# Kernel optimization log

Measured on AMD Instinct MI355X. Metric: run time of the kernel, lower is better.

The kernel has to match this reference:

```python
import jax, jax.numpy as jnp
import numpy as np

NUM_GRAPHS = 256
BN_EPS = 1e-5
GN_EPS = 1e-5


def setup_inputs() -> dict:
    key = jax.random.key(0)
    ks = jax.random.split(key, 8)
    N, E, D, H = 100000, 600000, 128, 128
    x = jax.random.normal(ks[0], (N, D), dtype=jnp.float32)
    W1 = jax.random.normal(ks[1], (4, 4 * H, D), dtype=jnp.float32) * 0.05
    bn_g = jnp.ones((4, 4 * H), dtype=jnp.float32)
    bn_b = jnp.zeros((4, 4 * H), dtype=jnp.float32)
    W2 = jax.random.normal(ks[2], (4, H, 4 * H), dtype=jnp.float32) * 0.05
    b2 = jnp.zeros((4, H), dtype=jnp.float32)
    gn_g = jnp.ones((4, H), dtype=jnp.float32)
    gn_b = jnp.zeros((4, H), dtype=jnp.float32)
    gn_a = jnp.ones((4, H), dtype=jnp.float32)
    edge_index = jax.random.randint(ks[3], (2, E), 0, N, dtype=jnp.int64)
    batch = jnp.sort(jax.random.randint(ks[4], (N,), 0, NUM_GRAPHS, dtype=jnp.int64))
    return {"x": x, "W1": W1, "bn_g": bn_g, "bn_b": bn_b, "W2": W2, "b2": b2,
            "gn_g": gn_g, "gn_b": gn_b, "gn_a": gn_a,
            "edge_index": edge_index, "batch": batch}


def reference(x, W1, bn_g, bn_b, W2, b2, gn_g, gn_b, gn_a, edge_index, batch):
    N = x.shape[0]
    src, dst = edge_index[0], edge_index[1]
    # per-graph node counts (shared by GraphNorm and mean-pool)
    cnt = jax.ops.segment_sum(jnp.ones((N,), x.dtype), batch, num_segments=NUM_GRAPHS)
    cnt = jnp.maximum(cnt, 1.0)[:, None]  # [G,1]

    h = x
    hs = []
    for l in range(4):  # fixed small layer loop
        # GINConv: (1+eps)*x + sum_{j->i} x_j, eps=0 default
        agg = jax.ops.segment_sum(h[src], dst, num_segments=N)
        z = h + agg
        # MLP: Linear(no bias) -> BatchNorm1d (batch stats) -> SELU -> Linear
        z = z @ W1[l].T
        mu = jnp.mean(z, axis=0)
        var = jnp.mean((z - mu) ** 2, axis=0)
        z = (z - mu) * jax.lax.rsqrt(var + BN_EPS) * bn_g[l] + bn_b[l]
        z = jax.nn.selu(z)
        z = z @ W2[l].T + b2[l]
        # GraphNorm: per-graph mean/var with learnable mean scale alpha
        gmean = jax.ops.segment_sum(z, batch, num_segments=NUM_GRAPHS) / cnt
        sub = z - gn_a[l] * gmean[batch]
        gvar = jax.ops.segment_sum(sub * sub, batch, num_segments=NUM_GRAPHS) / cnt
        z = gn_g[l] * sub * jax.lax.rsqrt(gvar[batch] + GN_EPS) + gn_b[l]
        z = jax.nn.selu(z)  # self.act (SELU, matching MLP)
        hs.append(z)
        h = z

    hg = jnp.concatenate(hs, axis=1)  # [N, 4*H]
    pooled = jax.ops.segment_sum(hg, batch, num_segments=NUM_GRAPHS) / cnt
    return pooled
```

## Files before the change

kernel.cpp:

```cpp
#include <hip/hip_runtime.h>
#include <hip/hip_bf16.h>


typedef __attribute__((ext_vector_type(8))) short bf16x8;
typedef __attribute__((ext_vector_type(4))) float f32x4;

#define MOMB 256

__device__ __forceinline__ unsigned short f2b(float x){
    __hip_bfloat16 h = __float2bfloat16(x);
    return *reinterpret_cast<unsigned short*>(&h);
}
__device__ __forceinline__ float b2f(unsigned short u){
    __hip_bfloat16 h;
    *reinterpret_cast<unsigned short*>(&h) = u;
    return __bfloat162float(h);
}
__device__ __forceinline__ float selu_f(float x){
    const float sc = 1.0507009873554805f, al = 1.6732632423543772f;
    return x > 0.f ? sc * x : sc * al * (__expf(x) - 1.f);
}

__global__ void count_kernel(const int* __restrict__ dst, int* __restrict__ counts, int E){
    int e = blockIdx.x * 256 + threadIdx.x;
    if (e < E) atomicAdd(&counts[dst[e]], 1);
}

__global__ void cnt_bs_kernel(const int* __restrict__ batch, float* __restrict__ cnt, int N){
    __shared__ int sb[257];
    int g = threadIdx.x;
    int lo = 0, hi = N;
    while (lo < hi){ int mid = (lo + hi) >> 1; if (batch[mid] < g) lo = mid + 1; else hi = mid; }
    sb[g] = lo;
    if (g == 0) sb[256] = N;
    __syncthreads();
    cnt[g] = fmaxf((float)(sb[g + 1] - sb[g]), 1.f);
}

__global__ __launch_bounds__(1024) void scan_kernel(const int* __restrict__ counts,
                                                    int* __restrict__ row_ptr, int N){
    __shared__ int wsum[16];
    __shared__ int wpre[16];
    __shared__ int s_total;
    __shared__ int s_running;
    int tid = threadIdx.x;
    int lane = tid & 63, wid = tid >> 6;
    if (tid == 0) s_running = 0;
    __syncthreads();
    for (int base = 0; base < N; base += 4096){
        int idx0 = base + tid * 4;
        int v[4];
        #pragma unroll
        for (int j = 0; j < 4; j++) v[j] = (idx0 + j < N) ? counts[idx0 + j] : 0;
        int tsum = v[0] + v[1] + v[2] + v[3];
        int x = tsum;
        #pragma unroll
        for (int off = 1; off < 64; off <<= 1){
            int y = __shfl_up(x, off, 64);
            if (lane >= off) x += y;
        }
        if (lane == 63) wsum[wid] = x;
        __syncthreads();
        if (wid == 0 && lane < 16){
            int w = wsum[lane];
            int xx = w;
            #pragma unroll
            for (int off = 1; off < 16; off <<= 1){
                int y = __shfl_up(xx, off, 64);
                if (lane >= off) xx += y;
            }
            wpre[lane] = xx - w;
            if (lane == 15) s_total = xx;
        }
        __syncthreads();
        int run = s_running + wpre[wid] + (x - tsum);
        #pragma unroll
        for (int j = 0; j < 4; j++){
            if (idx0 + j < N) row_ptr[idx0 + j] = run;
            run += v[j];
        }
        __syncthreads();
        if (tid == 0) s_running += s_total;
        __syncthreads();
    }
    if (tid == 0) row_ptr[N] = s_running;
}

__global__ void fill_kernel(const int* __restrict__ ei, const int* __restrict__ row_ptr,
                            int* __restrict__ fill, int* __restrict__ colv, int E){
    int e = blockIdx.x * 256 + threadIdx.x;
    if (e < E){
        int s = ei[e];
        int d = ei[E + e];
        int pos = atomicAdd(&fill[d], 1);
        colv[row_ptr[d] + pos] = s;
    }
}

__global__ void pack_kernel(const float* __restrict__ W1, const float* __restrict__ W2,
                            unsigned short* __restrict__ W1p, unsigned short* __restrict__ W2p){
    int t = blockIdx.x * 256 + threadIdx.x;
    int which = t >> 15;
    int u = t & 32767;
    int lane = u & 63; u >>= 6;
    int nf = u & 3; u >>= 2;
    int wc = u & 1; u >>= 1;
    int kk = u & 3; u >>= 2;
    int c = u & 3; u >>= 2;
    int l = u;
    int col = wc * 64 + nf * 16 + (lane & 15);
    int kbase = kk * 32 + (lane >> 4) * 8;
    size_t ob = ((((((size_t)(l * 4 + c) * 4 + kk) * 2 + wc) * 4 + nf) * 2) * 512) + lane * 8;
    unsigned short* dst = which == 0 ? W1p : W2p;
    #pragma unroll
    for (int j = 0; j < 8; j++){
        int k = kbase + j;
        float wv = which == 0 ? W1[((size_t)(l * 512) + c * 128 + col) * 128 + k]
                              : W2[((size_t)(l * 128) + col) * 512 + c * 128 + k];
        unsigned short hi = f2b(wv);
        unsigned short lo = f2b(wv - b2f(hi));
        dst[ob + j] = hi;
        dst[ob + 512 + j] = lo;
    }
}

__global__ __launch_bounds__(256) void agg_split_kernel(
    const float* __restrict__ h, const int* __restrict__ row_ptr,
    const int* __restrict__ colv,
    unsigned short* __restrict__ zhi, unsigned short* __restrict__ zlo, int N)
{
    int t = blockIdx.x * 256 + threadIdx.x;
    int i = t >> 5;
    if (i >= N) return;
    int vo = (t & 31);
    const float4* hv = reinterpret_cast<const float4*>(h);
    int p0 = row_ptr[i], p1 = row_ptr[i + 1];
    float4 acc = hv[(size_t)i * 32 + vo];
    int p = p0;
    for (; p + 4 <= p1; p += 4){
        int s0 = colv[p], s1 = colv[p + 1], s2 = colv[p + 2], s3 = colv[p + 3];
        float4 a = hv[(size_t)s0 * 32 + vo];
        float4 b = hv[(size_t)s1 * 32 + vo];
        float4 c = hv[(size_t)s2 * 32 + vo];
        float4 d = hv[(size_t)s3 * 32 + vo];
        acc.x += (a.x + b.x) + (c.x + d.x);
        acc.y += (a.y + b.y) + (c.y + d.y);
        acc.z += (a.z + b.z) + (c.z + d.z);
        acc.w += (a.w + b.w) + (c.w + d.w);
    }
    for (; p < p1; p++){
        float4 a = hv[(size_t)colv[p] * 32 + vo];
        acc.x += a.x; acc.y += a.y; acc.z += a.z; acc.w += a.w;
    }
    float vals[4] = {acc.x, acc.y, acc.z, acc.w};
    unsigned int h01, h23, l01, l23;
    {
        unsigned short hh[4], ll[4];
        #pragma unroll
        for (int j = 0; j < 4; j++){
            hh[j] = f2b(vals[j]);
            ll[j] = f2b(vals[j] - b2f(hh[j]));
        }
        h01 = (unsigned int)hh[0] | ((unsigned int)hh[1] << 16);
        h23 = (unsigned int)hh[2] | ((unsigned int)hh[3] << 16);
        l01 = (unsigned int)ll[0] | ((unsigned int)ll[1] << 16);
        l23 = (unsigned int)ll[2] | ((unsigned int)ll[3] << 16);
    }
    int kk = vo >> 3, kg = (vo >> 1) & 3, half = vo & 1;
    size_t fo = ((size_t)(i >> 4) * 4 + kk) * 512 + (kg * 16 + (i & 15)) * 8 + half * 4;
    *reinterpret_cast<uint2*>(zhi + fo) = make_uint2(h01, h23);
    *reinterpret_cast<uint2*>(zlo + fo) = make_uint2(l01, l23);
}

__device__ __forceinline__ bf16x8 tread(const unsigned short* __restrict__ s, int base){
    union { bf16x8 v; unsigned short u[8]; } r;
    #pragma unroll
    for (int j = 0; j < 8; j++) r.u[j] = s[base + j * 8];
    return r.v;
}

__global__ __launch_bounds__(256) void moment_k(
    const unsigned short* __restrict__ Zhi_g, const unsigned short* __restrict__ Zlo_g,
    float* __restrict__ Mpart, float* __restrict__ cpart, int RB)
{
    __shared__ __align__(16) unsigned short Zh_s[16384];
    __shared__ __align__(16) unsigned short Zl_s[16384];
    __shared__ float cs[256];
    int tid = threadIdx.x, lane = tid & 63, w = tid >> 6;
    int fl = lane & 15, g = lane >> 4;
    int tpart = (g >> 1) * 2048 + (g & 1) * 64;
    int fpart = (fl >> 3) * 128 + (fl & 7);

    f32x4 acc[2][8];
    #pragma unroll
    for (int i = 0; i < 2; i++)
        #pragma unroll
        for (int j = 0; j < 8; j++) acc[i][j] = (f32x4){0.f, 0.f, 0.f, 0.f};
    float csum = 0.f;
    int cf = tid & 127, chalf = tid >> 7;
    int cfbase = (cf >> 5) * 512 + ((cf >> 3) & 3) * 128 + (cf & 7);

    for (int blk = blockIdx.x; blk < RB; blk += MOMB){
        __syncthreads();
        {
            size_t gbase = (size_t)blk * 16384;
            const uint4* gh = reinterpret_cast<const uint4*>(Zhi_g + gbase);
            const uint4* gl = reinterpret_cast<const uint4*>(Zlo_g + gbase);
            uint4* sh4 = reinterpret_cast<uint4*>(Zh_s);
            uint4* sl4 = reinterpret_cast<uint4*>(Zl_s);
            #pragma unroll
            for (int j = 0; j < 8; j++){
                sh4[j * 256 + tid] = gh[j * 256 + tid];
                sl4[j * 256 + tid] = gl[j * 256 + tid];
            }
        }
        __syncthreads();

        #pragma unroll 8
        for (int n = chalf * 64; n < chalf * 64 + 64; n++){
            int addr = (n >> 4) * 2048 + (n & 15) * 8 + cfbase;
            csum += b2f(Zh_s[addr]) + b2f(Zl_s[addr]);
        }

        for (int nk = 0; nk < 4; nk++){
            int nb = nk * 4096 + tpart + fpart;
            bf16x8 ath[2], atl[2];
            #pragma unroll
            for (int i = 0; i < 2; i++){
                int ft = w * 2 + i;
                int base = nb + (ft >> 1) * 512 + (ft & 1) * 256;
                ath[i] = tread(Zh_s, base);
                atl[i] = tread(Zl_s, base);
            }
            #pragma unroll
            for (int ft2 = 0; ft2 < 8; ft2++){
                int base2 = nb + (ft2 >> 1) * 512 + (ft2 & 1) * 256;
                bf16x8 bth = tread(Zh_s, base2);
                bf16x8 btl = tread(Zl_s, base2);
                #pragma unroll
                for (int i = 0; i < 2; i++){
                    acc[i][ft2] = __builtin_amdgcn_mfma_f32_16x16x32_bf16(ath[i], bth, acc[i][ft2], 0, 0, 0);
                    acc[i][ft2] = __builtin_amdgcn_mfma_f32_16x16x32_bf16(ath[i], btl, acc[i][ft2], 0, 0, 0);
                    acc[i][ft2] = __builtin_amdgcn_mfma_f32_16x16x32_bf16(atl[i], bth, acc[i][ft2], 0, 0, 0);
                }
            }
        }
    }

    float* Mp = Mpart + (size_t)blockIdx.x * 16384;
    int col = lane & 15, rbase = (lane >> 4) * 4;
    #pragma unroll
    for (int i = 0; i < 2; i++)
        #pragma unroll
        for (int ft2 = 0; ft2 < 8; ft2++)
            #pragma unroll
            for (int r = 0; r < 4; r++){
                int a = (w * 2 + i) * 16 + rbase + r;
                int b = ft2 * 16 + col;
                Mp[a * 128 + b] = acc[i][ft2][r];
            }
    cs[tid] = csum;
    __syncthreads();
    if (tid < 128) cpart[(size_t)blockIdx.x * 128 + tid] = cs[tid] + cs[tid + 128];
}

__global__ __launch_bounds__(256) void reduce_k(
    const float* __restrict__ Mpart, const float* __restrict__ cpart,
    float* __restrict__ Msum, float* __restrict__ colsum)
{
    int gid = blockIdx.x * 256 + threadIdx.x;
    float s = 0.f;
    for (int p = 0; p < MOMB; p++) s += Mpart[(size_t)p * 16384 + gid];
    Msum[gid] = s;
    if (blockIdx.x == 0 && threadIdx.x < 128){
        float c = 0.f;
        for (int p = 0; p < MOMB; p++) c += cpart[(size_t)p * 128 + threadIdx.x];
        colsum[threadIdx.x] = c;
    }
}

__global__ __launch_bounds__(128) void bn_final2_k(
    const float* __restrict__ Msum, const float* __restrict__ colsum,
    const float* __restrict__ W1, const float* __restrict__ bng,
    const float* __restrict__ bnb, float* __restrict__ sc, float* __restrict__ sh,
    int l, float invN)
{
    __shared__ float s_w[128];
    __shared__ float red[4];
    int j = blockIdx.x;
    int t = threadIdx.x;
    float wt = W1[(size_t)l * 65536 + (size_t)j * 128 + t];
    s_w[t] = wt;
    __syncthreads();
    float y = 0.f;
    #pragma unroll 4
    for (int k = 0; k < 128; k++) y = fmaf(Msum[t * 128 + k], s_w[k], y);
    float p = wt * y;
    float mc = wt * colsum[t];
    #pragma unroll
    for (int off = 32; off >= 1; off >>= 1){
        p += __shfl_xor(p, off, 64);
        mc += __shfl_xor(mc, off, 64);
    }
    int lane = t & 63, wv = t >> 6;
    if (lane == 0){ red[wv * 2] = p; red[wv * 2 + 1] = mc; }
    __syncthreads();
    if (t == 0){
        float e2 = (red[0] + red[2]) * invN;
        float mu = (red[1] + red[3]) * invN;
        float var = e2 - mu * mu;
        float inv = rsqrtf(var + 1e-5f);
        float gg = bng[l * 512 + j] * inv;
        sc[j] = gg;
        sh[j] = bnb[l * 512 + j] - mu * gg;
    }
}

__global__ __launch_bounds__(512, 4) void fused_k(
    const unsigned short* __restrict__ Zhi_g, const unsigned short* __restrict__ Zlo_g,
    const unsigned short* __restrict__ B1p, const unsigned short* __restrict__ B2p,
    float* __restrict__ Z, const float* __restrict__ bsc, const float* __restrict__ bsh,
    const float* __restrict__ b2l, const int* __restrict__ batch,
    float* __restrict__ gsum, float* __restrict__ gsq, int N)
{
    __shared__ __align__(16) unsigned short Zh_s[8192];
    __shared__ __align__(16) unsigned short Zl_s[8192];
    __shared__ __align__(16) unsigned short Ph[64][136];
    __shared__ __align__(16) unsigned short Pl[64][136];
    __shared__ float s_sc[512], s_sh[512];
    __shared__ int s_b[64];
    int tid = threadIdx.x, lane = tid & 63, w = tid >> 6;
    int wr = w >> 2, wq = w & 3;
    int r_lo = lane & 15, kg = lane >> 4;
    int m0 = blockIdx.x * 64;

    if (tid < 512){ s_sc[tid] = bsc[tid]; s_sh[tid] = bsh[tid]; }
    if (tid < 64) s_b[tid] = (m0 + tid < N) ? batch[m0 + tid] : -1;
    {
        size_t gbase = (size_t)(m0 >> 4) * 2048;
        const uint4* gh = reinterpret_cast<const uint4*>(Zhi_g + gbase);
        const uint4* gl = reinterpret_cast<const uint4*>(Zlo_g + gbase);
        uint4* sh4 = reinterpret_cast<uint4*>(Zh_s);
        uint4* sl4 = reinterpret_cast<uint4*>(Zl_s);
        #pragma unroll
        for (int j = 0; j < 2; j++){
            sh4[j * 512 + tid] = gh[j * 512 + tid];
            sl4[j * 512 + tid] = gl[j * 512 + tid];
        }
    }
    __syncthreads();

    int wc = wq >> 1;
    f32x4 acc2[2][2];
    #pragma unroll
    for (int i = 0; i < 2; i++)
        #pragma unroll
        for (int j = 0; j < 2; j++) acc2[i][j] = (f32x4){0.f, 0.f, 0.f, 0.f};

    for (int c = 0; c < 4; c++){
        f32x4 acc1[2][2];
        #pragma unroll
        for (int i = 0; i < 2; i++)
            #pragma unroll
            for (int j = 0; j < 2; j++) acc1[i][j] = (f32x4){0.f, 0.f, 0.f, 0.f};

        const bf16x8* B1v = reinterpret_cast<const bf16x8*>(B1p) + (size_t)c * 4096;
        for (int kk = 0; kk < 4; kk++){
            bf16x8 awh[2], awl[2];
            #pragma unroll
            for (int mfp = 0; mfp < 2; mfp++){
                int colblk = wq * 2 + mfp;
                int wc1 = colblk >> 2, nf1 = colblk & 3;
                int ob = ((kk * 2 + wc1) * 4 + nf1) * 2;
                awh[mfp] = B1v[(ob + 0) * 64 + lane];
                awl[mfp] = B1v[(ob + 1) * 64 + lane];
            }
            bf16x8 bzh[2], bzl[2];
            #pragma unroll
            for (int nfp = 0; nfp < 2; nfp++){
                int so = ((wr * 2 + nfp) * 4 + kk) * 512 + lane * 8;
                bzh[nfp] = *reinterpret_cast<const bf16x8*>(&Zh_s[so]);
                bzl[nfp] = *reinterpret_cast<const bf16x8*>(&Zl_s[so]);
            }
            #pragma unroll
            for (int mfp = 0; mfp < 2; mfp++)
                #pragma unroll
                for (int nfp = 0; nfp < 2; nfp++){
                    acc1[mfp][nfp] = __builtin_amdgcn_mfma_f32_16x16x32_bf16(awh[mfp], bzh[nfp], acc1[mfp][nfp], 0, 0, 0);
                    acc1[mfp][nfp] = __builtin_amdgcn_mfma_f32_16x16x32_bf16(awh[mfp], bzl[nfp], acc1[mfp][nfp], 0, 0, 0);
                    acc1[mfp][nfp] = __builtin_amdgcn_mfma_f32_16x16x32_bf16(awl[mfp], bzh[nfp], acc1[mfp][nfp], 0, 0, 0);
                }
        }

        __syncthreads();
        #pragma unroll
        for (int mfp = 0; mfp < 2; mfp++){
            int ckb = wq * 32 + mfp * 16 + kg * 4;
            float sc0 = s_sc[c * 128 + ckb + 0], sh0 = s_sh[c * 128 + ckb + 0];
            float sc1 = s_sc[c * 128 + ckb + 1], sh1 = s_sh[c * 128 + ckb + 1];
            float sc2 = s_sc[c * 128 + ckb + 2], sh2 = s_sh[c * 128 + ckb + 2];
            float sc3 = s_sc[c * 128 + ckb + 3], sh3 = s_sh[c * 128 + ckb + 3];
            #pragma unroll
            for (int nfp = 0; nfp < 2; nfp++){
                float t0 = selu_f(fmaf(acc1[mfp][nfp][0], sc0, sh0));
                float t1 = selu_f(fmaf(acc1[mfp][nfp][1], sc1, sh1));
                float t2 = selu_f(fmaf(acc1[mfp][nfp][2], sc2, sh2));
                float t3 = selu_f(fmaf(acc1[mfp][nfp][3], sc3, sh3));
                unsigned short h0 = f2b(t0), h1 = f2b(t1), h2 = f2b(t2), h3 = f2b(t3);
                unsigned short l0 = f2b(t0 - b2f(h0)), l1 = f2b(t1 - b2f(h1));
                unsigned short l2 = f2b(t2 - b2f(h2)), l3 = f2b(t3 - b2f(h3));
                int node = wr * 32 + nfp * 16 + r_lo;
                uint2 hv = make_uint2((unsigned int)h0 | ((unsigned int)h1 << 16),
                                      (unsigned int)h2 | ((unsigned int)h3 << 16));
                uint2 lv = make_uint2((unsigned int)l0 | ((unsigned int)l1 << 16),
                                      (unsigned int)l2 | ((unsigned int)l3 << 16));
                *reinterpret_cast<uint2*>(&Ph[node][ckb]) = hv;
                *reinterpret_cast<uint2*>(&Pl[node][ckb]) = lv;
            }
        }
        __syncthreads();

        const bf16x8* B2v = reinterpret_cast<const bf16x8*>(B2p);
        for (int kk2 = 0; kk2 < 4; kk2++){
            int kkf = c * 4 + kk2;
            bf16x8 bh[2], bl[2];
            #pragma unroll
            for (int nf = 0; nf < 2; nf++){
                int nfold = (wq & 1) * 2 + nf;
                int ob = ((kkf * 2 + wc) * 4 + nfold) * 2;
                bh[nf] = B2v[(ob + 0) * 64 + lane];
                bl[nf] = B2v[(ob + 1) * 64 + lane];
            }
            bf16x8 ah[2], alr[2];
            #pragma unroll
            for (int mf = 0; mf < 2; mf++){
                int ar = wr * 32 + mf * 16 + r_lo;
                ah[mf]  = *reinterpret_cast<const bf16x8*>(&Ph[ar][kk2 * 32 + kg * 8]);
                alr[mf] = *reinterpret_cast<const bf16x8*>(&Pl[ar][kk2 * 32 + kg * 8]);
            }
            #pragma unroll
            for (int mf = 0; mf < 2; mf++)
                #pragma unroll
                for (int nf = 0; nf < 2; nf++){
                    acc2[mf][nf] = __builtin_amdgcn_mfma_f32_16x16x32_bf16(ah[mf],  bh[nf], acc2[mf][nf], 0, 0, 0);
                    acc2[mf][nf] = __builtin_amdgcn_mfma_f32_16x16x32_bf16(ah[mf],  bl[nf], acc2[mf][nf], 0, 0, 0);
                    acc2[mf][nf] = __builtin_amdgcn_mfma_f32_16x16x32_bf16(alr[mf], bh[nf], acc2[mf][nf], 0, 0, 0);
                }
        }
    }

    #pragma unroll
    for (int nf = 0; nf < 2; nf++){
        int col = wq * 32 + nf * 16 + r_lo;
        float bv = b2l[col];
        float s = 0.f, q = 0.f;
        int run_g = -2;
        #pragma unroll
        for (int mf = 0; mf < 2; mf++)
            #pragma unroll
            for (int r = 0; r < 4; r++){
                int row_l = wr * 32 + mf * 16 + kg * 4 + r;
                int row = m0 + row_l;
                if (row < N){
                    float v = bv + acc2[mf][nf][r];
                    Z[(size_t)row * 128 + col] = v;
                    int g = s_b[row_l];
                    if (g != run_g){
                        if (run_g >= 0){
                            atomicAdd(&gsum[run_g * 128 + col], s);
                            atomicAdd(&gsq[run_g * 128 + col], q);
                        }
                        s = 0.f; q = 0.f; run_g = g;
                    }
                    s += v; q += v * v;
                }
            }
        if (run_g >= 0){
            atomicAdd(&gsum[run_g * 128 + col], s);
            atomicAdd(&gsq[run_g * 128 + col], q);
        }
    }
}

__global__ void gn_final_kernel(float* __restrict__ gsum, float* __restrict__ gsq,
                                const float* __restrict__ cnt,
                                const float* __restrict__ gng, const float* __restrict__ gnb,
                                const float* __restrict__ gna,
                                float* __restrict__ scale, float* __restrict__ shift, int l){
    int g = blockIdx.x, c = threadIdx.x;
    int idx = g * 128 + c;
    float n = cnt[g];
    float m = gsum[idx] / n;
    float e2 = gsq[idx] / n;
    float a = gna[l * 128 + c];
    float var = e2 - (2.f * a - a * a) * m * m;
    float inv = rsqrtf(var + 1e-5f);
    float sc = gng[l * 128 + c] * inv;
    scale[idx] = sc;
    shift[idx] = gnb[l * 128 + c] - a * m * sc;
    gsum[idx] = 0.f;
    gsq[idx] = 0.f;
}

__global__ __launch_bounds__(256) void gn_apply_kernel(
    float* __restrict__ z2h, const int* __restrict__ batch,
    const float* __restrict__ scale, const float* __restrict__ shift,
    float* __restrict__ pool, int l, int N)
{
    __shared__ int sb[128];
    int tid = threadIdx.x;
    int base = blockIdx.x * 128;
    int end = min(128, N - base);
    if (tid < 128) sb[tid] = (tid < end) ? batch[base + tid] : 0;
    __syncthreads();
    int vo = tid & 31;
    int r0 = (tid >> 5) * 16;
    if (r0 >= end) return;
    int rend = min(r0 + 16, end);
    float4* zv = reinterpret_cast<float4*>(z2h);
    int run_g = sb[r0];
    float scx = scale[run_g * 128 + vo * 4 + 0], shx = shift[run_g * 128 + vo * 4 + 0];
    float scy = scale[run_g * 128 + vo * 4 + 1], shy = shift[run_g * 128 + vo * 4 + 1];
    float scz = scale[run_g * 128 + vo * 4 + 2], shz = shift[run_g * 128 + vo * 4 + 2];
    float scw = scale[run_g * 128 + vo * 4 + 3], shw = shift[run_g * 128 + vo * 4 + 3];
    float px = 0.f, py = 0.f, pz = 0.f, pw = 0.f;
    for (int r = r0; r < rend; r++){
        int g = sb[r];
        if (g != run_g){
            float* pp = &pool[run_g * 512 + l * 128 + vo * 4];
            atomicAdd(pp + 0, px); atomicAdd(pp + 1, py); atomicAdd(pp + 2, pz); atomicAdd(pp + 3, pw);
            px = py = pz = pw = 0.f;
            run_g = g;
            scx = scale[g * 128 + vo * 4 + 0]; shx = shift[g * 128 + vo * 4 + 0];
            scy = scale[g * 128 + vo * 4 + 1]; shy = shift[g * 128 + vo * 4 + 1];
            scz = scale[g * 128 + vo * 4 + 2]; shz = shift[g * 128 + vo * 4 + 2];
            scw = scale[g * 128 + vo * 4 + 3]; shw = shift[g * 128 + vo * 4 + 3];
        }
        size_t idx = (size_t)(base + r) * 32 + vo;
        float4 v = zv[idx];
        v.x = selu_f(fmaf(v.x, scx, shx));
        v.y = selu_f(fmaf(v.y, scy, shy));
        v.z = selu_f(fmaf(v.z, scz, shz));
        v.w = selu_f(fmaf(v.w, scw, shw));
        zv[idx] = v;
        px += v.x; py += v.y; pz += v.z; pw += v.w;
    }
    float* pp = &pool[run_g * 512 + l * 128 + vo * 4];
    atomicAdd(pp + 0, px); atomicAdd(pp + 1, py); atomicAdd(pp + 2, pz); atomicAdd(pp + 3, pw);
}

__global__ void final_kernel(const float* __restrict__ pool, const float* __restrict__ cnt,
                             float* __restrict__ out, int n){
    int i = blockIdx.x * 256 + threadIdx.x;
    if (i < n) out[i] = pool[i] / cnt[i >> 9];
}

extern "C" void kernel_launch(void* const* d_in, const int* in_sizes, int n_in,
                              void* d_out, int out_size, void* d_ws, size_t ws_size,
                              hipStream_t stream){
    const float* x    = (const float*)d_in[0];
    const float* W1   = (const float*)d_in[1];
    const float* bng  = (const float*)d_in[2];
    const float* bnb  = (const float*)d_in[3];
    const float* W2   = (const float*)d_in[4];
    const float* b2   = (const float*)d_in[5];
    const float* gng  = (const float*)d_in[6];
    const float* gnb  = (const float*)d_in[7];
    const float* gna  = (const float*)d_in[8];
    const int*   ei   = (const int*)d_in[9];
    const int*   batch= (const int*)d_in[10];
    int N = in_sizes[0] / 128;
    int E = in_sizes[9] / 2;
    float* out = (float*)d_out;
    int RB = (N + 127) / 128;
    int RB64 = (N + 63) / 64;

    char* ws = (char*)d_ws;
    size_t off = 0;
    auto alloc = [&](size_t bytes) -> char* {
        char* p = ws + off;
        off += (bytes + 255) & ~(size_t)255;
        return p;
    };
    unsigned short* z0hi = (unsigned short*)alloc((size_t)RB * 128 * 128 * 2);
    unsigned short* z0lo = (unsigned short*)alloc((size_t)RB * 128 * 128 * 2);
    float* z2     = (float*)alloc((size_t)N * 128 * 4);
    unsigned short* W1p = (unsigned short*)alloc(524288 * 2);
    unsigned short* W2p = (unsigned short*)alloc(524288 * 2);
    int*   row_ptr= (int*)alloc((size_t)(N + 1) * 4);
    int*   colv   = (int*)alloc((size_t)E * 4);
    int*   counts = (int*)alloc((size_t)N * 4);
    int*   fill   = (int*)alloc((size_t)N * 4);
    float* cnt_f  = (float*)alloc(256 * 4);
    float* Mpart  = (float*)alloc((size_t)MOMB * 16384 * 4);
    float* cpart  = (float*)alloc((size_t)MOMB * 128 * 4);
    float* Msum   = (float*)alloc(16384 * 4);
    float* colsum = (float*)alloc(128 * 4);
    float* bn_sc  = (float*)alloc(512 * 4);
    float* bn_sh  = (float*)alloc(512 * 4);
    float* gn_sum = (float*)alloc(256 * 128 * 4);
    float* gn_sq  = (float*)alloc(256 * 128 * 4);
    float* gn_sc  = (float*)alloc(256 * 128 * 4);
    float* gn_sh  = (float*)alloc(256 * 128 * 4);
    float* pool   = (float*)alloc(256 * 512 * 4);
    (void)ws_size;

    hipMemsetAsync(counts, 0, (size_t)N * 4, stream);
    hipMemsetAsync(fill,   0, (size_t)N * 4, stream);
    hipMemsetAsync(gn_sum, 0, 2 * 256 * 128 * 4, stream);
    hipMemsetAsync(pool,   0, 256 * 512 * 4, stream);
    {
        size_t tail_start = (size_t)(N >> 4) * 2048;
        size_t total      = (size_t)RB * 128 * 128;
        if (total > tail_start){
            size_t tail_bytes = (total - tail_start) * 2;
            hipMemsetAsync(z0hi + tail_start, 0, tail_bytes, stream);
            hipMemsetAsync(z0lo + tail_start, 0, tail_bytes, stream);
        }
    }

    pack_kernel<<<256, 256, 0, stream>>>(W1, W2, W1p, W2p);
    count_kernel<<<(E + 255) / 256, 256, 0, stream>>>(ei + E, counts, E);
    scan_kernel<<<1, 1024, 0, stream>>>(counts, row_ptr, N);
    fill_kernel<<<(E + 255) / 256, 256, 0, stream>>>(ei, row_ptr, fill, colv, E);
    cnt_bs_kernel<<<1, 256, 0, stream>>>(batch, cnt_f, N);

    const float* hcur = x;
    float invN = 1.f / (float)N;
    for (int l = 0; l < 4; l++){
        agg_split_kernel<<<(N + 7) / 8, 256, 0, stream>>>(hcur, row_ptr, colv, z0hi, z0lo, N);
        moment_k<<<MOMB, 256, 0, stream>>>(z0hi, z0lo, Mpart, cpart, RB);
        reduce_k<<<64, 256, 0, stream>>>(Mpart, cpart, Msum, colsum);
        bn_final2_k<<<512, 128, 0, stream>>>(Msum, colsum, W1, bng, bnb,
                                             bn_sc, bn_sh, l, invN);
        fused_k<<<RB64, 512, 0, stream>>>(z0hi, z0lo, W1p + (size_t)l * 131072,
                                          W2p + (size_t)l * 131072, z2,
                                          bn_sc, bn_sh, b2 + l * 128,
                                          batch, gn_sum, gn_sq, N);
        gn_final_kernel<<<256, 128, 0, stream>>>(gn_sum, gn_sq, cnt_f, gng, gnb, gna,
                                                 gn_sc, gn_sh, l);
        gn_apply_kernel<<<RB, 256, 0, stream>>>(z2, batch, gn_sc, gn_sh, pool, l, N);
        hcur = z2;
    }
    final_kernel<<<(out_size + 255) / 256, 256, 0, stream>>>(pool, cnt_f, out, out_size);
}
```

Baseline: 1.306 ms.

## Fuse GraphNorm apply and pooling into next layer's neighbor aggregation

Removes the separate GraphNorm-apply pass that read and rewrote z2 each layer. The next layer's aggregation kernel now applies the per-graph scale/shift and SELU on the fly to each gathered neighbor and to the node itself, and accumulates the pooled sum. This saves a full read-modify-write of the N×128 activation per layer. The cost is recomputing the normalisation and SELU once per edge, with extra batch and scale/shift gathers per neighbor. A standalone pool kernel handles the last layer.

```diff
diff --git a/kernel.cpp b/kernel.cpp
--- a/kernel.cpp
+++ b/kernel.cpp
@@ -172,6 +172,147 @@
     *reinterpret_cast<uint2*>(zlo + fo) = make_uint2(l01, l23);
 }
 
+__global__ __launch_bounds__(256) void agg_tx_kernel(
+    const float* __restrict__ z2, const int* __restrict__ row_ptr,
+    const int* __restrict__ colv, const int* __restrict__ batch,
+    const float* __restrict__ scale, const float* __restrict__ shift,
+    unsigned short* __restrict__ zhi, unsigned short* __restrict__ zlo,
+    float* __restrict__ pool, int lpool, int N)
+{
+    __shared__ float pbuf[8][128];
+    __shared__ int s_g[8];
+    int tid = threadIdx.x;
+    int t = blockIdx.x * 256 + tid;
+    int i = t >> 5;
+    int vo = t & 31;
+    int il = tid >> 5;
+    if (vo == 0) s_g[il] = (i < N) ? batch[i] : -1;
+    const float4* hv = reinterpret_cast<const float4*>(z2);
+    float4 acc = make_float4(0.f, 0.f, 0.f, 0.f);
+    if (i < N){
+        int gi = batch[i];
+        float4 v  = hv[(size_t)i * 32 + vo];
+        float4 c4 = *reinterpret_cast<const float4*>(&scale[gi * 128 + vo * 4]);
+        float4 s4 = *reinterpret_cast<const float4*>(&shift[gi * 128 + vo * 4]);
+        acc.x = selu_f(fmaf(v.x, c4.x, s4.x));
+        acc.y = selu_f(fmaf(v.y, c4.y, s4.y));
+        acc.z = selu_f(fmaf(v.z, c4.z, s4.z));
+        acc.w = selu_f(fmaf(v.w, c4.w, s4.w));
+        pbuf[il][vo * 4 + 0] = acc.x;
+        pbuf[il][vo * 4 + 1] = acc.y;
+        pbuf[il][vo * 4 + 2] = acc.z;
+        pbuf[il][vo * 4 + 3] = acc.w;
+    }
+    __syncthreads();
+    if (tid < 128){
+        float s = 0.f; int rg = -2;
+        #pragma unroll
+        for (int k = 0; k < 8; k++){
+            int g = s_g[k];
+            if (g < 0) continue;
+            if (g != rg){
+                if (rg >= 0) atomicAdd(&pool[rg * 512 + lpool * 128 + tid], s);
+                s = 0.f; rg = g;
+            }
+            s += pbuf[k][tid];
+        }
+        if (rg >= 0) atomicAdd(&pool[rg * 512 + lpool * 128 + tid], s);
+    }
+    if (i >= N) return;
+
+    int p0 = row_ptr[i], p1 = row_ptr[i + 1];
+    int p = p0;
+    for (; p + 2 <= p1; p += 2){
+        int s0 = colv[p], s1 = colv[p + 1];
+        int g0 = batch[s0], g1 = batch[s1];
+        float4 v0 = hv[(size_t)s0 * 32 + vo];
+        float4 v1 = hv[(size_t)s1 * 32 + vo];
+        float4 c0 = *reinterpret_cast<const float4*>(&scale[g0 * 128 + vo * 4]);
+        float4 h0 = *reinterpret_cast<const float4*>(&shift[g0 * 128 + vo * 4]);
+        float4 c1 = *reinterpret_cast<const float4*>(&scale[g1 * 128 + vo * 4]);
+        float4 h1 = *reinterpret_cast<const float4*>(&shift[g1 * 128 + vo * 4]);
+        acc.x += selu_f(fmaf(v0.x, c0.x, h0.x)) + selu_f(fmaf(v1.x, c1.x, h1.x));
+        acc.y += selu_f(fmaf(v0.y, c0.y, h0.y)) + selu_f(fmaf(v1.y, c1.y, h1.y));
+        acc.z += selu_f(fmaf(v0.z, c0.z, h0.z)) + selu_f(fmaf(v1.z, c1.z, h1.z));
+        acc.w += selu_f(fmaf(v0.w, c0.w, h0.w)) + selu_f(fmaf(v1.w, c1.w, h1.w));
+    }
+    for (; p < p1; p++){
+        int s0 = colv[p];
+        int g0 = batch[s0];
+        float4 v0 = hv[(size_t)s0 * 32 + vo];
+        float4 c0 = *reinterpret_cast<const float4*>(&scale[g0 * 128 + vo * 4]);
+        float4 h0 = *reinterpret_cast<const float4*>(&shift[g0 * 128 + vo * 4]);
+        acc.x += selu_f(fmaf(v0.x, c0.x, h0.x));
+        acc.y += selu_f(fmaf(v0.y, c0.y, h0.y));
+        acc.z += selu_f(fmaf(v0.z, c0.z, h0.z));
+        acc.w += selu_f(fmaf(v0.w, c0.w, h0.w));
+    }
+
+    float vals[4] = {acc.x, acc.y, acc.z, acc.w};
+    unsigned int h01, h23, l01, l23;
+    {
+        unsigned short hh[4], ll[4];
+        #pragma unroll
+        for (int j = 0; j < 4; j++){
+            hh[j] = f2b(vals[j]);
+            ll[j] = f2b(vals[j] - b2f(hh[j]));
+        }
+        h01 = (unsigned int)hh[0] | ((unsigned int)hh[1] << 16);
+        h23 = (unsigned int)hh[2] | ((unsigned int)hh[3] << 16);
+        l01 = (unsigned int)ll[0] | ((unsigned int)ll[1] << 16);
+        l23 = (unsigned int)ll[2] | ((unsigned int)ll[3] << 16);
+    }
+    int kk = vo >> 3, kg = (vo >> 1) & 3, half = vo & 1;
+    size_t fo = ((size_t)(i >> 4) * 4 + kk) * 512 + (kg * 16 + (i & 15)) * 8 + half * 4;
+    *reinterpret_cast<uint2*>(zhi + fo) = make_uint2(h01, h23);
+    *reinterpret_cast<uint2*>(zlo + fo) = make_uint2(l01, l23);
+}
+
+__global__ __launch_bounds__(256) void pool_tx_kernel(
+    const float* __restrict__ z2, const int* __restrict__ batch,
+    const float* __restrict__ scale, const float* __restrict__ shift,
+    float* __restrict__ pool, int l, int N)
+{
+    __shared__ int sb[128];
+    int tid = threadIdx.x;
+    int base = blockIdx.x * 128;
+    int end = min(128, N - base);
+    if (tid < 128) sb[tid] = (tid < end) ? batch[base + tid] : 0;
+    __syncthreads();
+    int vo = tid & 31;
+    int r0 = (tid >> 5) * 16;
+    if (r0 >= end) return;
+    int rend = min(r0 + 16, end);
+    const float4* zv = reinterpret_cast<const float4*>(z2);
+    int run_g = sb[r0];
+    float scx = scale[run_g * 128 + vo * 4 + 0], shx = shift[run_g * 128 + vo * 4 + 0];
+    float scy = scale[run_g * 128 + vo * 4 + 1], shy = shift[run_g * 128 + vo * 4 + 1];
+    float scz = scale[run_g * 128 + vo * 4 + 2], shz = shift[run_g * 128 + vo * 4 + 2];
+    float scw = scale[run_g * 128 + vo * 4 + 3], shw = shift[run_g * 128 + vo * 4 + 3];
+    float px = 0.f, py = 0.f, pz = 0.f, pw = 0.f;
+    for (int r = r0; r < rend; r++){
+        int g = sb[r];
+        if (g != run_g){
+            float* pp = &pool[run_g * 512 + l * 128 + vo * 4];
+            atomicAdd(pp + 0, px); atomicAdd(pp + 1, py); atomicAdd(pp + 2, pz); atomicAdd(pp + 3, pw);
+            px = py = pz = pw = 0.f;
+            run_g = g;
+            scx = scale[g * 128 + vo * 4 + 0]; shx = shift[g * 128 + vo * 4 + 0];
+            scy = scale[g * 128 + vo * 4 + 1]; shy = shift[g * 128 + vo * 4 + 1];
+            scz = scale[g * 128 + vo * 4 + 2]; shz = shift[g * 128 + vo * 4 + 2];
+            scw = scale[g * 128 + vo * 4 + 3]; shw = shift[g * 128 + vo * 4 + 3];
+        }
+        size_t idx = (size_t)(base + r) * 32 + vo;
+        float4 v = zv[idx];
+        px += selu_f(fmaf(v.x, scx, shx));
+        py += selu_f(fmaf(v.y, scy, shy));
+        pz += selu_f(fmaf(v.z, scz, shz));
+        pw += selu_f(fmaf(v.w, scw, shw));
+    }
+    float* pp = &pool[run_g * 512 + l * 128 + vo * 4];
+    atomicAdd(pp + 0, px); atomicAdd(pp + 1, py); atomicAdd(pp + 2, pz); atomicAdd(pp + 3, pw);
+}
+
 __device__ __forceinline__ bf16x8 tread(const unsigned short* __restrict__ s, int base){
     union { bf16x8 v; unsigned short u[8]; } r;
     #pragma unroll
@@ -500,53 +641,6 @@
     shift[idx] = gnb[l * 128 + c] - a * m * sc;
     gsum[idx] = 0.f;
     gsq[idx] = 0.f;
-}
-
-__global__ __launch_bounds__(256) void gn_apply_kernel(
-    float* __restrict__ z2h, const int* __restrict__ batch,
-    const float* __restrict__ scale, const float* __restrict__ shift,
-    float* __restrict__ pool, int l, int N)
-{
-    __shared__ int sb[128];
-    int tid = threadIdx.x;
-    int base = blockIdx.x * 128;
-    int end = min(128, N - base);
-    if (tid < 128) sb[tid] = (tid < end) ? batch[base + tid] : 0;
-    __syncthreads();
-    int vo = tid & 31;
-    int r0 = (tid >> 5) * 16;
-    if (r0 >= end) return;
-    int rend = min(r0 + 16, end);
-    float4* zv = reinterpret_cast<float4*>(z2h);
-    int run_g = sb[r0];
-    float scx = scale[run_g * 128 + vo * 4 + 0], shx = shift[run_g * 128 + vo * 4 + 0];
-    float scy = scale[run_g * 128 + vo * 4 + 1], shy = shift[run_g * 128 + vo * 4 + 1];
-    float scz = scale[run_g * 128 + vo * 4 + 2], shz = shift[run_g * 128 + vo * 4 + 2];
-    float scw = scale[run_g * 128 + vo * 4 + 3], shw = shift[run_g * 128 + vo * 4 + 3];
-    float px = 0.f, py = 0.f, pz = 0.f, pw = 0.f;
-    for (int r = r0; r < rend; r++){
-        int g = sb[r];
-        if (g != run_g){
-            float* pp = &pool[run_g * 512 + l * 128 + vo * 4];
-            atomicAdd(pp + 0, px); atomicAdd(pp + 1, py); atomicAdd(pp + 2, pz); atomicAdd(pp + 3, pw);
-            px = py = pz = pw = 0.f;
-            run_g = g;
-            scx = scale[g * 128 + vo * 4 + 0]; shx = shift[g * 128 + vo * 4 + 0];
-            scy = scale[g * 128 + vo * 4 + 1]; shy = shift[g * 128 + vo * 4 + 1];
-            scz = scale[g * 128 + vo * 4 + 2]; shz = shift[g * 128 + vo * 4 + 2];
-            scw = scale[g * 128 + vo * 4 + 3]; shw = shift[g * 128 + vo * 4 + 3];
-        }
-        size_t idx = (size_t)(base + r) * 32 + vo;
-        float4 v = zv[idx];
-        v.x = selu_f(fmaf(v.x, scx, shx));
-        v.y = selu_f(fmaf(v.y, scy, shy));
-        v.z = selu_f(fmaf(v.z, scz, shz));
-        v.w = selu_f(fmaf(v.w, scw, shw));
-        zv[idx] = v;
-        px += v.x; py += v.y; pz += v.z; pw += v.w;
-    }
-    float* pp = &pool[run_g * 512 + l * 128 + vo * 4];
-    atomicAdd(pp + 0, px); atomicAdd(pp + 1, py); atomicAdd(pp + 2, pz); atomicAdd(pp + 3, pw);
 }
 
 __global__ void final_kernel(const float* __restrict__ pool, const float* __restrict__ cnt,
@@ -625,10 +719,15 @@
     fill_kernel<<<(E + 255) / 256, 256, 0, stream>>>(ei, row_ptr, fill, colv, E);
     cnt_bs_kernel<<<1, 256, 0, stream>>>(batch, cnt_f, N);
 
-    const float* hcur = x;
     float invN = 1.f / (float)N;
     for (int l = 0; l < 4; l++){
-        agg_split_kernel<<<(N + 7) / 8, 256, 0, stream>>>(hcur, row_ptr, colv, z0hi, z0lo, N);
+        if (l == 0)
+            agg_split_kernel<<<(N + 7) / 8, 256, 0, stream>>>(x, row_ptr, colv,
+                                                              z0hi, z0lo, N);
+        else
+            agg_tx_kernel<<<(N + 7) / 8, 256, 0, stream>>>(z2, row_ptr, colv, batch,
+                                                           gn_sc, gn_sh, z0hi, z0lo,
+                                                           pool, l - 1, N);
         moment_k<<<MOMB, 256, 0, stream>>>(z0hi, z0lo, Mpart, cpart, RB);
         reduce_k<<<64, 256, 0, stream>>>(Mpart, cpart, Msum, colsum);
         bn_final2_k<<<512, 128, 0, stream>>>(Msum, colsum, W1, bng, bnb,
@@ -639,8 +738,7 @@
                                           batch, gn_sum, gn_sq, N);
         gn_final_kernel<<<256, 128, 0, stream>>>(gn_sum, gn_sq, cnt_f, gng, gnb, gna,
                                                  gn_sc, gn_sh, l);
-        gn_apply_kernel<<<RB, 256, 0, stream>>>(z2, batch, gn_sc, gn_sh, pool, l, N);
-        hcur = z2;
-    }
+    }
+    pool_tx_kernel<<<RB, 256, 0, stream>>>(z2, batch, gn_sc, gn_sh, pool, 3, N);
     final_kernel<<<(out_size + 255) / 256, 256, 0, stream>>>(pool, cnt_f, out, out_size);
 }
```

New measurement: 1.268 ms, median of 2. -2.9%, faster.
